# Optimization experiments

Hardware: AMD Instinct MI355X
Metric: run time of the kernel (lower is better)

## Reference

```python
import jax, jax.numpy as jnp
import numpy as np

N = 50000      # nodes
E = 800000     # edges (avg degree 16)
D_IN = 16      # raw node feature dim
D = 64         # d_model
H = 8          # heads
DH = D // H    # dim_head = 8
L = 2          # num_encoder_layers
EPS = 1e-5
SCALE = float(np.sqrt(DH))


def _xavier(key, shape):
    fan_in, fan_out = shape[-2], shape[-1]
    a = float(np.sqrt(6.0 / (fan_in + fan_out)))
    return jax.random.uniform(key, shape, jnp.float32, -a, a)


def setup_inputs() -> dict:
    key = jax.random.key(0)
    ks = jax.random.split(key, 20)
    feat = jax.random.normal(ks[0], (N, D_IN), jnp.float32)
    src = jax.random.randint(ks[1], (E,), 0, N, jnp.int32)
    dst = jax.random.randint(ks[2], (E,), 0, N, jnp.int32)
    return {
        "feat": feat,
        "src": src,
        "dst": dst,
        "W_emb": _xavier(ks[3], (D_IN, D)),
        "b_emb": jnp.zeros((D,), jnp.float32),
        "Wq": _xavier(ks[4], (L, D, D)),
        "Wk": _xavier(ks[5], (L, D, D)),
        "Wv": _xavier(ks[6], (L, D, D)),
        "Wo": _xavier(ks[7], (L, D, D)),
        "bo": jnp.zeros((L, D), jnp.float32),
        "bn1_g": jnp.ones((L, D), jnp.float32),
        "bn1_b": jnp.zeros((L, D), jnp.float32),
        "W1": _xavier(ks[8], (L, D, 2 * D)),
        "b1": jnp.zeros((L, 2 * D), jnp.float32),
        "W2": _xavier(ks[9], (L, 2 * D, D)),
        "b2": jnp.zeros((L, D), jnp.float32),
        "bn2_g": jnp.ones((L, D), jnp.float32),
        "bn2_b": jnp.zeros((L, D), jnp.float32),
    }


def _batch_norm(x, g, b):
    # BatchNorm1d (training-mode forward: batch statistics, biased var)
    mu = jnp.mean(x, axis=0)
    var = jnp.var(x, axis=0)
    return (x - mu) / jnp.sqrt(var + EPS) * g + b


def _layer(h, src, dst, Wq, Wk, Wv, Wo, bo, bn1_g, bn1_b, W1, b1, W2, b2, bn2_g, bn2_b):
    h_in1 = h
    Q = (h @ Wq).reshape(N, H, DH)
    K = (h @ Wk).reshape(N, H, DH)
    V = (h @ Wv).reshape(N, H, DH)
    # SDDMM: per-edge dot(K[src], Q[dst]) -> [E, H]
    e = jnp.sum(K[src] * Q[dst], axis=-1)
    # scaled_exp: exp(clamp(score/sqrt(dh), -10, 10)) stored as edge 'score'
    e = jnp.exp(jnp.clip(e / SCALE, -10.0, 10.0))
    # reduce_func then applies a softmax over mailbox scores (double exp, faithful)
    m = jax.ops.segment_max(e, dst, num_segments=N)          # [N, H]
    w = jnp.exp(e - m[dst])                                   # [E, H]
    s = jax.ops.segment_sum(w, dst, num_segments=N)           # [N, H]
    alpha = w / s[dst]                                        # [E, H]
    out = jax.ops.segment_sum(alpha[:, :, None] * V[src], dst, num_segments=N)
    h = out.reshape(N, D) @ Wo + bo
    h = _batch_norm(h_in1 + h, bn1_g, bn1_b)
    h_in2 = h
    h = jax.nn.relu(h @ W1 + b1) @ W2 + b2
    h = _batch_norm(h + h_in2, bn2_g, bn2_b)
    return h


def reference(feat, src, dst, W_emb, b_emb, Wq, Wk, Wv, Wo, bo, bn1_g, bn1_b,
              W1, b1, W2, b2, bn2_g, bn2_b):
    h = feat @ W_emb + b_emb  # embedding_h (dropout=0)
    for l in range(L):
        h = _layer(h, src, dst, Wq[l], Wk[l], Wv[l], Wo[l], bo[l],
                   bn1_g[l], bn1_b[l], W1[l], b1[l], W2[l], b2[l],
                   bn2_g[l], bn2_b[l])
    return h
```

## Files before the change

### kernel.cpp

```cpp
#include <hip/hip_runtime.h>

#define NNODES 50000
#define NEDGES 800000
#define DM 64
#define NH 8
#define DH 8
#define EPSN 1e-5f
#define INV_SCALE 0.3535533905932738f
#define SCAN_BLOCKS 200
#define SCAN_CHUNK  250

template<int KA, int KB, int R, bool RELU, bool RES, bool STATS, bool BNRES>
__global__ __launch_bounds__(256, 2) void gemm_k(const float* __restrict__ A,
    const float* __restrict__ W, int woff,
    const float* __restrict__ bias, int boff,
    float* __restrict__ C, float* __restrict__ stats,
    const float* __restrict__ bnstats, const float* __restrict__ bng, int bgoff,
    const float* __restrict__ bnb, int bboff, int Nrows)
{
    constexpr int CG   = KB / 4;
    constexpr int RG   = 256 / CG;
    constexpr int ROWS = RG * R;
    constexpr int APAD = KA + 4;
    constexpr int KAq  = KA / 4;

    __shared__ __align__(16) float sW[KA * KB];
    __shared__ __align__(16) float sA[ROWS * APAD];

    const int tid  = threadIdx.x;
    const int row0 = blockIdx.x * ROWS;

    for (int i4 = tid; i4 < KA * KB / 4; i4 += 256)
        *(float4*)&sW[i4 * 4] = ((const float4*)(W + woff))[i4];
    for (int i4 = tid; i4 < ROWS * KAq; i4 += 256) {
        int r = i4 / KAq, kq = i4 - r * KAq;
        int gr = row0 + r;
        float4 v = make_float4(0.f, 0.f, 0.f, 0.f);
        if (gr < Nrows) v = ((const float4*)A)[(size_t)gr * KAq + kq];
        *(float4*)&sA[r * APAD + kq * 4] = v;
    }
    __syncthreads();

    const int cg = tid % CG, rg = tid / CG;
    const int c0 = cg * 4, r0 = rg * R;

    float4 acc[R];
#pragma unroll
    for (int rr = 0; rr < R; rr++) acc[rr] = make_float4(0.f, 0.f, 0.f, 0.f);

#pragma unroll 2
    for (int k = 0; k < KA; k += 4) {
        float4 w0 = *(const float4*)&sW[(k + 0) * KB + c0];
        float4 w1 = *(const float4*)&sW[(k + 1) * KB + c0];
        float4 w2 = *(const float4*)&sW[(k + 2) * KB + c0];
        float4 w3 = *(const float4*)&sW[(k + 3) * KB + c0];
#pragma unroll
        for (int rr = 0; rr < R; rr++) {
            float4 av = *(const float4*)&sA[(r0 + rr) * APAD + k];
            acc[rr].x += av.x * w0.x + av.y * w1.x + av.z * w2.x + av.w * w3.x;
            acc[rr].y += av.x * w0.y + av.y * w1.y + av.z * w2.y + av.w * w3.y;
            acc[rr].z += av.x * w0.z + av.y * w1.z + av.z * w2.z + av.w * w3.z;
            acc[rr].w += av.x * w0.w + av.y * w1.w + av.z * w2.w + av.w * w3.w;
        }
    }

    float4 bv = make_float4(0.f, 0.f, 0.f, 0.f);
    if (bias) {
        bv.x = bias[boff + c0];     bv.y = bias[boff + c0 + 1];
        bv.z = bias[boff + c0 + 2]; bv.w = bias[boff + c0 + 3];
    }

    float4 scR = make_float4(1.f, 1.f, 1.f, 1.f);
    float4 ofR = make_float4(0.f, 0.f, 0.f, 0.f);
    if (BNRES) {
        const float inv_n = 1.0f / NNODES;
#pragma unroll
        for (int j = 0; j < 4; j++) {
            float mu   = bnstats[c0 + j] * inv_n;
            float var  = bnstats[KB + c0 + j] * inv_n - mu * mu;
            float istd = rsqrtf(fmaxf(var, 0.f) + EPSN);
            float s    = istd * bng[bgoff + c0 + j];
            ((float*)&scR)[j] = s;
            ((float*)&ofR)[j] = bnb[bboff + c0 + j] - mu * s;
        }
    }

    float4 vals[R];
#pragma unroll
    for (int rr = 0; rr < R; rr++) {
        int grow = row0 + r0 + rr;
        bool valid = grow < Nrows;
        float4 v;
        v.x = acc[rr].x + bv.x; v.y = acc[rr].y + bv.y;
        v.z = acc[rr].z + bv.z; v.w = acc[rr].w + bv.w;
        if (RELU) {
            v.x = fmaxf(v.x, 0.f); v.y = fmaxf(v.y, 0.f);
            v.z = fmaxf(v.z, 0.f); v.w = fmaxf(v.w, 0.f);
        }
        if (valid) {
            if (RES) {
                float4 old = *(const float4*)&C[(size_t)grow * KB + c0];
                if (BNRES) {
                    old.x = old.x * scR.x + ofR.x;
                    old.y = old.y * scR.y + ofR.y;
                    old.z = old.z * scR.z + ofR.z;
                    old.w = old.w * scR.w + ofR.w;
                }
                v.x += old.x; v.y += old.y; v.z += old.z; v.w += old.w;
            }
            *(float4*)&C[(size_t)grow * KB + c0] = v;
        } else {
            v = make_float4(0.f, 0.f, 0.f, 0.f);
        }
        vals[rr] = v;
    }

    if (STATS) {
        __syncthreads();
        float4 cs = make_float4(0.f, 0.f, 0.f, 0.f);
#pragma unroll
        for (int rr = 0; rr < R; rr++) {
            cs.x += vals[rr].x; cs.y += vals[rr].y;
            cs.z += vals[rr].z; cs.w += vals[rr].w;
        }
        *(float4*)&sA[rg * KB + c0] = cs;
        __syncthreads();
        if (tid < KB) {
            float s = 0.f;
#pragma unroll
            for (int g = 0; g < RG; g++) s += sA[g * KB + tid];
            atomicAdd(&stats[tid], s);
        }
        __syncthreads();
        float4 cq = make_float4(0.f, 0.f, 0.f, 0.f);
#pragma unroll
        for (int rr = 0; rr < R; rr++) {
            cq.x += vals[rr].x * vals[rr].x; cq.y += vals[rr].y * vals[rr].y;
            cq.z += vals[rr].z * vals[rr].z; cq.w += vals[rr].w * vals[rr].w;
        }
        *(float4*)&sA[rg * KB + c0] = cq;
        __syncthreads();
        if (tid < KB) {
            float s = 0.f;
#pragma unroll
            for (int g = 0; g < RG; g++) s += sA[g * KB + tid];
            atomicAdd(&stats[KB + tid], s);
        }
    }
}

template<bool BNIN>
__global__ __launch_bounds__(256, 2) void qkv_k(const float* __restrict__ A,
    const float* __restrict__ Wq, const float* __restrict__ Wk,
    const float* __restrict__ Wv, int woff,
    float* __restrict__ Qo, float* __restrict__ Ko, float* __restrict__ Vo,
    const float* __restrict__ bnstats, const float* __restrict__ bng, int bgoff,
    const float* __restrict__ bnb, int bboff, int Nrows)
{
    constexpr int APAD = 68;
    __shared__ __align__(16) float sW[64 * 64];
    __shared__ __align__(16) float sA[64 * APAD];

    const int tid  = threadIdx.x;
    const int row0 = blockIdx.x * 64;

    {
        const int kq = tid & 15, cc = kq * 4;
        float4 sc = make_float4(1.f, 1.f, 1.f, 1.f);
        float4 of = make_float4(0.f, 0.f, 0.f, 0.f);
        if (BNIN) {
            const float inv_n = 1.0f / NNODES;
#pragma unroll
            for (int j = 0; j < 4; j++) {
                float mu   = bnstats[cc + j] * inv_n;
                float var  = bnstats[64 + cc + j] * inv_n - mu * mu;
                float istd = rsqrtf(fmaxf(var, 0.f) + EPSN);
                float s    = istd * bng[bgoff + cc + j];
                ((float*)&sc)[j] = s;
                ((float*)&of)[j] = bnb[bboff + cc + j] - mu * s;
            }
        }
        for (int i4 = tid; i4 < 64 * 16; i4 += 256) {
            int r = i4 >> 4;
            int gr = row0 + r;
            float4 v = make_float4(0.f, 0.f, 0.f, 0.f);
            if (gr < Nrows) {
                v = ((const float4*)A)[(size_t)gr * 16 + kq];
                if (BNIN) {
                    v.x = v.x * sc.x + of.x; v.y = v.y * sc.y + of.y;
                    v.z = v.z * sc.z + of.z; v.w = v.w * sc.w + of.w;
                }
            }
            *(float4*)&sA[r * APAD + cc] = v;
        }
    }

    const float* Ws[3]   = {Wq, Wk, Wv};
    float*       Outs[3] = {Qo, Ko, Vo};

    const int cg = tid & 15, rg = tid >> 4;
    const int c0 = cg * 4, r0 = rg * 4;

    for (int m = 0; m < 3; m++) {
        __syncthreads();
        for (int i4 = tid; i4 < 1024; i4 += 256)
            *(float4*)&sW[i4 * 4] = ((const float4*)(Ws[m] + woff))[i4];
        __syncthreads();

        float4 acc[4];
#pragma unroll
        for (int rr = 0; rr < 4; rr++) acc[rr] = make_float4(0.f, 0.f, 0.f, 0.f);

#pragma unroll 2
        for (int k = 0; k < 64; k += 4) {
            float4 w0 = *(const float4*)&sW[(k + 0) * 64 + c0];
            float4 w1 = *(const float4*)&sW[(k + 1) * 64 + c0];
            float4 w2 = *(const float4*)&sW[(k + 2) * 64 + c0];
            float4 w3 = *(const float4*)&sW[(k + 3) * 64 + c0];
#pragma unroll
            for (int rr = 0; rr < 4; rr++) {
                float4 av = *(const float4*)&sA[(r0 + rr) * APAD + k];
                acc[rr].x += av.x * w0.x + av.y * w1.x + av.z * w2.x + av.w * w3.x;
                acc[rr].y += av.x * w0.y + av.y * w1.y + av.z * w2.y + av.w * w3.y;
                acc[rr].z += av.x * w0.z + av.y * w1.z + av.z * w2.z + av.w * w3.z;
                acc[rr].w += av.x * w0.w + av.y * w1.w + av.z * w2.w + av.w * w3.w;
            }
        }

#pragma unroll
        for (int rr = 0; rr < 4; rr++) {
            int grow = row0 + r0 + rr;
            if (grow < Nrows)
                *(float4*)&Outs[m][(size_t)grow * 64 + c0] = acc[rr];
        }
    }
}

__global__ __launch_bounds__(256, 4) void ffn_k(float* __restrict__ H,
    const float* __restrict__ W1, int w1off,
    const float* __restrict__ b1, int b1off,
    const float* __restrict__ W2, int w2off,
    const float* __restrict__ b2, int b2off,
    const float* __restrict__ bnstats,
    const float* __restrict__ bng, int bgoff,
    const float* __restrict__ bnb, int bboff,
    float* __restrict__ stats2, int Nrows)
{
    constexpr int APAD = 68;
    __shared__ __align__(16) float sA[4][8 * APAD];
    __shared__ __align__(16) float sF[4][8 * 128];
    __shared__ __align__(16) float sR[4 * 64];

    const int tid  = threadIdx.x;
    const int w    = tid >> 6;
    const int c    = tid & 63;
    const int row0 = blockIdx.x * 32 + w * 8;

    float* sAw = sA[w];
    float* sFw = sF[w];
    const float* __restrict__ W1g = W1 + w1off;
    const float* __restrict__ W2g = W2 + w2off;

    {
        const int q = c & 15;
        const int r = c >> 4;
        const float inv_n = 1.0f / NNODES;
        float4 sc, of;
#pragma unroll
        for (int j = 0; j < 4; j++) {
            float mu   = bnstats[q * 4 + j] * inv_n;
            float var  = bnstats[64 + q * 4 + j] * inv_n - mu * mu;
            float istd = rsqrtf(fmaxf(var, 0.f) + EPSN);
            float s    = istd * bng[bgoff + q * 4 + j];
            ((float*)&sc)[j] = s;
            ((float*)&of)[j] = bnb[bboff + q * 4 + j] - mu * s;
        }
#pragma unroll
        for (int rr = 0; rr < 2; rr++) {
            int lr = r + rr * 4;
            int gr = row0 + lr;
            float4 v = make_float4(0.f, 0.f, 0.f, 0.f);
            if (gr < Nrows) {
                v = ((const float4*)H)[(size_t)gr * 16 + q];
                v.x = v.x * sc.x + of.x; v.y = v.y * sc.y + of.y;
                v.z = v.z * sc.z + of.z; v.w = v.w * sc.w + of.w;
            }
            *(float4*)&sAw[lr * APAD + q * 4] = v;
        }
    }

    {
        float accL[8], accH[8];
#pragma unroll
        for (int r = 0; r < 8; r++) { accL[r] = 0.f; accH[r] = 0.f; }
#pragma unroll 2
        for (int k4 = 0; k4 < 16; k4++) {
            float4 av[8];
#pragma unroll
            for (int r = 0; r < 8; r++)
                av[r] = *(const float4*)&sAw[r * APAD + k4 * 4];
#pragma unroll
            for (int j = 0; j < 4; j++) {
                int k = k4 * 4 + j;
                float wl = W1g[k * 128 + c];
                float wh = W1g[k * 128 + c + 64];
#pragma unroll
                for (int r = 0; r < 8; r++) {
                    float a = ((const float*)&av[r])[j];
                    accL[r] += a * wl;
                    accH[r] += a * wh;
                }
            }
        }
        float bL = b1[b1off + c], bH = b1[b1off + c + 64];
#pragma unroll
        for (int r = 0; r < 8; r++) {
            sFw[r * 128 + c]      = fmaxf(accL[r] + bL, 0.f);
            sFw[r * 128 + c + 64] = fmaxf(accH[r] + bH, 0.f);
        }
    }

    float acc2[8];
#pragma unroll
    for (int r = 0; r < 8; r++) acc2[r] = 0.f;
#pragma unroll 2
    for (int k4 = 0; k4 < 32; k4++) {
        float4 fv[8];
#pragma unroll
        for (int r = 0; r < 8; r++)
            fv[r] = *(const float4*)&sFw[r * 128 + k4 * 4];
#pragma unroll
        for (int j = 0; j < 4; j++) {
            int k = k4 * 4 + j;
            float w2 = W2g[k * 64 + c];
#pragma unroll
            for (int r = 0; r < 8; r++)
                acc2[r] += ((const float*)&fv[r])[j] * w2;
        }
    }

    const float bc = b2[b2off + c];
    float vals[8];
#pragma unroll
    for (int r = 0; r < 8; r++) {
        int grow = row0 + r;
        float v = acc2[r] + bc + sAw[r * APAD + c];
        if (grow < Nrows) H[(size_t)grow * 64 + c] = v;
        else v = 0.f;
        vals[r] = v;
    }

    float s = 0.f, qsum = 0.f;
#pragma unroll
    for (int r = 0; r < 8; r++) { s += vals[r]; qsum += vals[r] * vals[r]; }
    sR[w * 64 + c] = s;
    __syncthreads();
    if (tid < 64) {
        float t = sR[tid] + sR[64 + tid] + sR[128 + tid] + sR[192 + tid];
        atomicAdd(&stats2[tid], t);
    }
    __syncthreads();
    sR[w * 64 + c] = qsum;
    __syncthreads();
    if (tid < 64) {
        float t = sR[tid] + sR[64 + tid] + sR[128 + tid] + sR[192 + tid];
        atomicAdd(&stats2[64 + tid], t);
    }
}

__global__ __launch_bounds__(256) void bn_apply(const float* __restrict__ Hin,
    float* __restrict__ Hout, const float* __restrict__ stats,
    const float* __restrict__ g, int goff, const float* __restrict__ b, int boff)
{
    int i = blockIdx.x * 256 + threadIdx.x;
    if (i >= NNODES * DM) return;
    int c = i & 63;
    float mu  = stats[c] * (1.0f / NNODES);
    float var = stats[64 + c] * (1.0f / NNODES) - mu * mu;
    float istd = rsqrtf(fmaxf(var, 0.0f) + EPSN);
    Hout[i] = (Hin[i] - mu) * istd * g[goff + c] + b[boff + c];
}

__global__ __launch_bounds__(256) void zero_int_k(int* __restrict__ p, int n)
{
    int i = blockIdx.x * 256 + threadIdx.x;
    if (i < n) p[i] = 0;
}

__global__ __launch_bounds__(256) void count_k(const int* __restrict__ dst,
                                               int* __restrict__ cursor)
{
    int e = blockIdx.x * 256 + threadIdx.x;
    if (e < NEDGES) atomicAdd(&cursor[dst[e]], 1);
}

__global__ __launch_bounds__(256) void csr_scanA(const int* __restrict__ cursor,
                                                 int* __restrict__ bsum)
{
    __shared__ int red[256];
    const int base = blockIdx.x * SCAN_CHUNK;
    int s = 0;
    for (int i = threadIdx.x; i < SCAN_CHUNK; i += 256) s += cursor[base + i];
    red[threadIdx.x] = s;
    __syncthreads();
    for (int o = 128; o > 0; o >>= 1) {
        if (threadIdx.x < o) red[threadIdx.x] += red[threadIdx.x + o];
        __syncthreads();
    }
    if (threadIdx.x == 0) bsum[blockIdx.x] = red[0];
}

__global__ __launch_bounds__(256) void csr_scanB(int* __restrict__ bsum)
{
    __shared__ int t[256];
    const int tid = threadIdx.x;
    int v = (tid < SCAN_BLOCKS) ? bsum[tid] : 0;
    t[tid] = v;
    __syncthreads();
    for (int off = 1; off < 256; off <<= 1) {
        int x = (tid >= off) ? t[tid - off] : 0;
        __syncthreads();
        t[tid] += x;
        __syncthreads();
    }
    if (tid < SCAN_BLOCKS) bsum[tid] = t[tid] - v;
}

__global__ __launch_bounds__(256) void csr_scanC(int* __restrict__ cursor,
    int* __restrict__ rowptr, const int* __restrict__ bsum)
{
    __shared__ int t[256];
    const int base = blockIdx.x * SCAN_CHUNK;
    const int tid  = threadIdx.x;
    int deg = (tid < SCAN_CHUNK) ? cursor[base + tid] : 0;
    t[tid] = deg;
    __syncthreads();
    for (int off = 1; off < 256; off <<= 1) {
        int x = (tid >= off) ? t[tid - off] : 0;
        __syncthreads();
        t[tid] += x;
        __syncthreads();
    }
    int excl = bsum[blockIdx.x] + t[tid] - deg;
    if (tid < SCAN_CHUNK) {
        rowptr[base + tid] = excl;
        cursor[base + tid] = excl;
    }
    if (blockIdx.x == 0 && tid == 0) rowptr[NNODES] = NEDGES;
}

__global__ __launch_bounds__(256) void fill_k(const int* __restrict__ src,
    const int* __restrict__ dst, int* __restrict__ cursor,
    int* __restrict__ nbr)
{
    int e = blockIdx.x * 256 + threadIdx.x;
    if (e >= NEDGES) return;
    int pos = atomicAdd(&cursor[dst[e]], 1);
    nbr[pos] = src[e];
}

__global__ __launch_bounds__(256) void attn_fused_k(const float* __restrict__ Q,
    const float* __restrict__ K, const float* __restrict__ V,
    const int* __restrict__ rowptr, const int* __restrict__ nbr,
    float* __restrict__ U)
{
    const int w = threadIdx.x >> 6;
    const int d = blockIdx.x * 4 + w;
    if (d >= NNODES) return;
    const int l  = threadIdx.x & 63;
    const int el = l >> 3;
    const int h  = l & 7;
    const int e0 = rowptr[d], e1 = rowptr[d + 1];
    const int deg = e1 - e0;

    if (deg == 0) {
        U[(size_t)d * DM + h * DH + el] = 0.f;
        return;
    }

    const float4* qp = (const float4*)(Q + (size_t)d * DM + h * DH);
    const float4 q0 = qp[0], q1 = qp[1];

    float m = 0.0f;
    float S = 0.0f;
    float u[8] = {0.f, 0.f, 0.f, 0.f, 0.f, 0.f, 0.f, 0.f};

    for (int base = 0; base < deg; base += 16) {
        const int i0 = base + el, i1 = base + 8 + el;
        const bool v0ok = i0 < deg, v1ok = i1 < deg;
        const int s0 = nbr[e0 + (v0ok ? i0 : 0)];
        const int s1 = nbr[e0 + (v1ok ? i1 : 0)];

        const float4* kp0 = (const float4*)(K + (size_t)s0 * DM + h * DH);
        const float4* vp0 = (const float4*)(V + (size_t)s0 * DM + h * DH);
        const float4* kp1 = (const float4*)(K + (size_t)s1 * DM + h * DH);
        const float4* vp1 = (const float4*)(V + (size_t)s1 * DM + h * DH);
        float4 ka0 = kp0[0], ka1 = kp0[1];
        float4 kb0 = kp1[0], kb1 = kp1[1];
        float4 va0 = vp0[0], va1 = vp0[1];
        float4 vb0 = vp1[0], vb1 = vp1[1];

        float d0 = ka0.x * q0.x + ka0.y * q0.y + ka0.z * q0.z + ka0.w * q0.w
                 + ka1.x * q1.x + ka1.y * q1.y + ka1.z * q1.z + ka1.w * q1.w;
        float d1 = kb0.x * q0.x + kb0.y * q0.y + kb0.z * q0.z + kb0.w * q0.w
                 + kb1.x * q1.x + kb1.y * q1.y + kb1.z * q1.z + kb1.w * q1.w;

        float ev0 = __expf(fminf(fmaxf(d0 * INV_SCALE, -10.f), 10.f));
        float ev1 = __expf(fminf(fmaxf(d1 * INV_SCALE, -10.f), 10.f));
        if (!v0ok) ev0 = 0.f;
        if (!v1ok) ev1 = 0.f;

        float bm = fmaxf(ev0, ev1);
        bm = fmaxf(bm, __shfl_xor(bm, 8, 64));
        bm = fmaxf(bm, __shfl_xor(bm, 16, 64));
        bm = fmaxf(bm, __shfl_xor(bm, 32, 64));

        const float mn = fmaxf(m, bm);
        const float r  = __expf(m - mn);
        const float w0 = v0ok ? __expf(ev0 - mn) : 0.f;
        const float w1 = v1ok ? __expf(ev1 - mn) : 0.f;

        S = S * r + w0 + w1;
        u[0] = u[0] * r + w0 * va0.x + w1 * vb0.x;
        u[1] = u[1] * r + w0 * va0.y + w1 * vb0.y;
        u[2] = u[2] * r + w0 * va0.z + w1 * vb0.z;
        u[3] = u[3] * r + w0 * va0.w + w1 * vb0.w;
        u[4] = u[4] * r + w0 * va1.x + w1 * vb1.x;
        u[5] = u[5] * r + w0 * va1.y + w1 * vb1.y;
        u[6] = u[6] * r + w0 * va1.z + w1 * vb1.z;
        u[7] = u[7] * r + w0 * va1.w + w1 * vb1.w;
        m = mn;
    }

#pragma unroll
    for (int off = 8; off <= 32; off <<= 1) {
        S += __shfl_xor(S, off, 64);
#pragma unroll
        for (int j = 0; j < 8; j++) u[j] += __shfl_xor(u[j], off, 64);
    }

    const float out = (S > 0.f) ? u[el] / S : 0.f;
    U[(size_t)d * DM + h * DH + el] = out;
}

__global__ __launch_bounds__(256) void fill_const_k(float* __restrict__ out, int n)
{
    int i = blockIdx.x * 256 + threadIdx.x;
    if (i < n) out[i] = 100.0f;
}

extern "C" void kernel_launch(void* const* d_in, const int* in_sizes, int n_in,
                              void* d_out, int out_size, void* d_ws, size_t ws_size,
                              hipStream_t stream)
{
    const int expect[18] = {800000, 800000, 800000, 1024, 64,
                            8192, 8192, 8192, 8192, 128,
                            128, 128, 16384, 256, 16384, 128, 128, 128};
    bool order_ok = (n_in == 18) && (out_size == NNODES * DM);
    if (order_ok)
        for (int i = 0; i < 18; i++)
            if (in_sizes[i] != expect[i]) { order_ok = false; break; }
    if (!order_ok) {
        fill_const_k<<<(out_size + 255) / 256, 256, 0, stream>>>((float*)d_out,
                                                                 out_size);
        return;
    }

    const float* feat  = (const float*)d_in[0];
    const int*   src   = (const int*)d_in[1];
    const int*   dst   = (const int*)d_in[2];
    const float* W_emb = (const float*)d_in[3];
    const float* b_emb = (const float*)d_in[4];
    const float* Wq    = (const float*)d_in[5];
    const float* Wk    = (const float*)d_in[6];
    const float* Wv    = (const float*)d_in[7];
    const float* Wo    = (const float*)d_in[8];
    const float* bo    = (const float*)d_in[9];
    const float* bn1_g = (const float*)d_in[10];
    const float* bn1_b = (const float*)d_in[11];
    const float* W1    = (const float*)d_in[12];
    const float* b1    = (const float*)d_in[13];
    const float* W2    = (const float*)d_in[14];
    const float* b2    = (const float*)d_in[15];
    const float* bn2_g = (const float*)d_in[16];
    const float* bn2_b = (const float*)d_in[17];

    const size_t ND = (size_t)NNODES * DM;
    float* ws     = (float*)d_ws;
    float* Hb     = ws;
    float* Qb     = Hb + ND;
    float* Kb     = Qb + ND;
    float* Vb     = Kb + ND;
    float* Ub     = Vb + ND;
    float* stats  = Ub + ND;
    int*   rowptr = (int*)(stats + 256);
    int*   cursor = rowptr + (NNODES + 1);
    int*   bsum   = cursor + NNODES;
    int*   nbr    = bsum + SCAN_BLOCKS;

    float* statsA = stats;
    float* statsB = stats + 128;

    const size_t BASE = (5 * ND + 256) * 4
                      + ((NNODES + 1) + NNODES + SCAN_BLOCKS + NEDGES) * 4;
    if (ws_size < BASE) {
        fill_const_k<<<(out_size + 255) / 256, 256, 0, stream>>>((float*)d_out,
                                                                 out_size);
        return;
    }

    const int g64 = (NNODES + 63) / 64;
    const int g32 = (NNODES + 31) / 32;
    const int gND = (int)(ND / 256);
    const int gE  = (NEDGES + 255) / 256;
    const int gAT = (NNODES + 3) / 4;

    zero_int_k<<<(NNODES + 255) / 256, 256, 0, stream>>>(cursor, NNODES);
    count_k<<<gE, 256, 0, stream>>>(dst, cursor);
    csr_scanA<<<SCAN_BLOCKS, 256, 0, stream>>>(cursor, bsum);
    csr_scanB<<<1, 256, 0, stream>>>(bsum);
    csr_scanC<<<SCAN_BLOCKS, 256, 0, stream>>>(cursor, rowptr, bsum);
    fill_k<<<gE, 256, 0, stream>>>(src, dst, cursor, nbr);

    gemm_k<16, 64, 4, false, false, false, false>
        <<<g64, 256, 0, stream>>>(feat, W_emb, 0, b_emb, 0, Hb, nullptr,
                                  nullptr, nullptr, 0, nullptr, 0, NNODES);

    for (int l = 0; l < 2; l++) {
        const int woff  = l * DM * DM;
        const int w1off = l * DM * 2 * DM;
        const int boff  = l * DM;
        const int b1off = l * 2 * DM;
        const int poff  = (l - 1) * DM;

        if (l == 0)
            qkv_k<false><<<g64, 256, 0, stream>>>(Hb, Wq, Wk, Wv, woff,
                Qb, Kb, Vb, nullptr, nullptr, 0, nullptr, 0, NNODES);
        else
            qkv_k<true><<<g64, 256, 0, stream>>>(Hb, Wq, Wk, Wv, woff,
                Qb, Kb, Vb, statsB, bn2_g, poff, bn2_b, poff, NNODES);

        attn_fused_k<<<gAT, 256, 0, stream>>>(Qb, Kb, Vb, rowptr, nbr, Ub);

        hipMemsetAsync(statsA, 0, 128 * 4, stream);
        if (l == 0)
            gemm_k<64, 64, 4, false, true, true, false>
                <<<g64, 256, 0, stream>>>(Ub, Wo, woff, bo, boff, Hb, statsA,
                                          nullptr, nullptr, 0, nullptr, 0, NNODES);
        else
            gemm_k<64, 64, 4, false, true, true, true>
                <<<g64, 256, 0, stream>>>(Ub, Wo, woff, bo, boff, Hb, statsA,
                                          statsB, bn2_g, poff, bn2_b, poff, NNODES);

        hipMemsetAsync(statsB, 0, 128 * 4, stream);
        ffn_k<<<g32, 256, 0, stream>>>(Hb, W1, w1off, b1, b1off,
                                       W2, w1off, b2, boff,
                                       statsA, bn1_g, boff, bn1_b, boff,
                                       statsB, NNODES);
    }

    bn_apply<<<gND, 256, 0, stream>>>(Hb, (float*)d_out, statsB,
                                      bn2_g, DM, bn2_b, DM);
}
```

Before: 567.0 us.

## Remap FFN kernel threads to row-by-column-quad with float4 weight loads

Restructures the fused FFN kernel so each lane owns one row and four adjacent output columns, not one column across eight rows. Weight reads become float4 vector loads, the hidden buffer gets padding, and the per-column stats reduction uses wavefront shuffles with a single barrier and one combined atomic pass. This aims to cut global load instruction count and barrier overhead, but gives up the reuse of each weight value across eight rows. Per-thread weight traffic therefore rises, and the BN scale/offset is now recomputed per element.

```diff
diff --git a/kernel.cpp b/kernel.cpp
--- a/kernel.cpp
+++ b/kernel.cpp
@@ -247,124 +247,123 @@
     float* __restrict__ stats2, int Nrows)
 {
     constexpr int APAD = 68;
-    __shared__ __align__(16) float sA[4][8 * APAD];
-    __shared__ __align__(16) float sF[4][8 * 128];
-    __shared__ __align__(16) float sR[4 * 64];
+    constexpr int FPAD = 132;
+    __shared__ __align__(16) float smem[2176 + 4224 + 512];
 
     const int tid  = threadIdx.x;
     const int w    = tid >> 6;
-    const int c    = tid & 63;
+    const int lane = tid & 63;
+    const int r    = lane >> 3;
+    const int j    = lane & 7;
     const int row0 = blockIdx.x * 32 + w * 8;
-
-    float* sAw = sA[w];
-    float* sFw = sF[w];
+    const int grow = row0 + r;
+    const bool rv  = grow < Nrows;
+
+    float* sAw = smem + w * (8 * APAD);
+    float* sFw = smem + 2176 + w * (8 * FPAD);
+    float* sR  = smem + 2176 + 4224;
+
     const float* __restrict__ W1g = W1 + w1off;
     const float* __restrict__ W2g = W2 + w2off;
 
     {
-        const int q = c & 15;
-        const int r = c >> 4;
         const float inv_n = 1.0f / NNODES;
-        float4 sc, of;
-#pragma unroll
-        for (int j = 0; j < 4; j++) {
-            float mu   = bnstats[q * 4 + j] * inv_n;
-            float var  = bnstats[64 + q * 4 + j] * inv_n - mu * mu;
-            float istd = rsqrtf(fmaxf(var, 0.f) + EPSN);
-            float s    = istd * bng[bgoff + q * 4 + j];
-            ((float*)&sc)[j] = s;
-            ((float*)&of)[j] = bnb[bboff + q * 4 + j] - mu * s;
-        }
-#pragma unroll
-        for (int rr = 0; rr < 2; rr++) {
-            int lr = r + rr * 4;
-            int gr = row0 + lr;
+#pragma unroll
+        for (int t = 0; t < 2; t++) {
+            const int q = j + t * 8;
             float4 v = make_float4(0.f, 0.f, 0.f, 0.f);
-            if (gr < Nrows) {
-                v = ((const float4*)H)[(size_t)gr * 16 + q];
-                v.x = v.x * sc.x + of.x; v.y = v.y * sc.y + of.y;
-                v.z = v.z * sc.z + of.z; v.w = v.w * sc.w + of.w;
-            }
-            *(float4*)&sAw[lr * APAD + q * 4] = v;
-        }
-    }
-
-    {
-        float accL[8], accH[8];
-#pragma unroll
-        for (int r = 0; r < 8; r++) { accL[r] = 0.f; accH[r] = 0.f; }
-#pragma unroll 2
-        for (int k4 = 0; k4 < 16; k4++) {
-            float4 av[8];
-#pragma unroll
-            for (int r = 0; r < 8; r++)
-                av[r] = *(const float4*)&sAw[r * APAD + k4 * 4];
-#pragma unroll
-            for (int j = 0; j < 4; j++) {
-                int k = k4 * 4 + j;
-                float wl = W1g[k * 128 + c];
-                float wh = W1g[k * 128 + c + 64];
-#pragma unroll
-                for (int r = 0; r < 8; r++) {
-                    float a = ((const float*)&av[r])[j];
-                    accL[r] += a * wl;
-                    accH[r] += a * wh;
+            if (rv) {
+                v = ((const float4*)H)[(size_t)grow * 16 + q];
+#pragma unroll
+                for (int jj = 0; jj < 4; jj++) {
+                    float mu   = bnstats[q * 4 + jj] * inv_n;
+                    float var  = bnstats[64 + q * 4 + jj] * inv_n - mu * mu;
+                    float istd = rsqrtf(fmaxf(var, 0.f) + EPSN);
+                    float s    = istd * bng[bgoff + q * 4 + jj];
+                    ((float*)&v)[jj] = ((float*)&v)[jj] * s
+                                     + (bnb[bboff + q * 4 + jj] - mu * s);
                 }
             }
-        }
-        float bL = b1[b1off + c], bH = b1[b1off + c + 64];
-#pragma unroll
-        for (int r = 0; r < 8; r++) {
-            sFw[r * 128 + c]      = fmaxf(accL[r] + bL, 0.f);
-            sFw[r * 128 + c + 64] = fmaxf(accH[r] + bH, 0.f);
-        }
-    }
-
-    float acc2[8];
-#pragma unroll
-    for (int r = 0; r < 8; r++) acc2[r] = 0.f;
-#pragma unroll 2
-    for (int k4 = 0; k4 < 32; k4++) {
-        float4 fv[8];
-#pragma unroll
-        for (int r = 0; r < 8; r++)
-            fv[r] = *(const float4*)&sFw[r * 128 + k4 * 4];
-#pragma unroll
-        for (int j = 0; j < 4; j++) {
-            int k = k4 * 4 + j;
-            float w2 = W2g[k * 64 + c];
-#pragma unroll
-            for (int r = 0; r < 8; r++)
-                acc2[r] += ((const float*)&fv[r])[j] * w2;
-        }
-    }
-
-    const float bc = b2[b2off + c];
-    float vals[8];
-#pragma unroll
-    for (int r = 0; r < 8; r++) {
-        int grow = row0 + r;
-        float v = acc2[r] + bc + sAw[r * APAD + c];
-        if (grow < Nrows) H[(size_t)grow * 64 + c] = v;
-        else v = 0.f;
-        vals[r] = v;
-    }
-
-    float s = 0.f, qsum = 0.f;
-#pragma unroll
-    for (int r = 0; r < 8; r++) { s += vals[r]; qsum += vals[r] * vals[r]; }
-    sR[w * 64 + c] = s;
+            *(float4*)&sAw[r * APAD + q * 4] = v;
+        }
+    }
+
+#pragma unroll
+    for (int p = 0; p < 4; p++) {
+        const int c0 = p * 32 + j * 4;
+        float4 acc = make_float4(0.f, 0.f, 0.f, 0.f);
+#pragma unroll 4
+        for (int k4 = 0; k4 < 16; k4++) {
+            float4 a = *(const float4*)&sAw[r * APAD + k4 * 4];
+#pragma unroll
+            for (int kk = 0; kk < 4; kk++) {
+                float av = ((const float*)&a)[kk];
+                float4 wv = *(const float4*)&W1g[(k4 * 4 + kk) * 128 + c0];
+                acc.x += av * wv.x; acc.y += av * wv.y;
+                acc.z += av * wv.z; acc.w += av * wv.w;
+            }
+        }
+        float4 bb = *(const float4*)&b1[b1off + c0];
+        acc.x = fmaxf(acc.x + bb.x, 0.f);
+        acc.y = fmaxf(acc.y + bb.y, 0.f);
+        acc.z = fmaxf(acc.z + bb.z, 0.f);
+        acc.w = fmaxf(acc.w + bb.w, 0.f);
+        *(float4*)&sFw[r * FPAD + c0] = acc;
+    }
+
+    float4 outv[2];
+#pragma unroll
+    for (int p = 0; p < 2; p++) {
+        const int c0 = p * 32 + j * 4;
+        float4 acc = make_float4(0.f, 0.f, 0.f, 0.f);
+#pragma unroll 4
+        for (int k4 = 0; k4 < 32; k4++) {
+            float4 f = *(const float4*)&sFw[r * FPAD + k4 * 4];
+#pragma unroll
+            for (int kk = 0; kk < 4; kk++) {
+                float fv = ((const float*)&f)[kk];
+                float4 wv = *(const float4*)&W2g[(k4 * 4 + kk) * 64 + c0];
+                acc.x += fv * wv.x; acc.y += fv * wv.y;
+                acc.z += fv * wv.z; acc.w += fv * wv.w;
+            }
+        }
+        float4 bb  = *(const float4*)&b2[b2off + c0];
+        float4 res = *(const float4*)&sAw[r * APAD + c0];
+        float4 v;
+        v.x = acc.x + bb.x + res.x;
+        v.y = acc.y + bb.y + res.y;
+        v.z = acc.z + bb.z + res.z;
+        v.w = acc.w + bb.w + res.w;
+        if (rv) *(float4*)&H[(size_t)grow * 64 + c0] = v;
+        else    v = make_float4(0.f, 0.f, 0.f, 0.f);
+        outv[p] = v;
+    }
+
+    float4 s0 = outv[0], s1 = outv[1];
+    float4 q0, q1;
+    q0.x = s0.x * s0.x; q0.y = s0.y * s0.y; q0.z = s0.z * s0.z; q0.w = s0.w * s0.w;
+    q1.x = s1.x * s1.x; q1.y = s1.y * s1.y; q1.z = s1.z * s1.z; q1.w = s1.w * s1.w;
+#pragma unroll
+    for (int off = 8; off <= 32; off <<= 1) {
+        s0.x += __shfl_xor(s0.x, off, 64); s0.y += __shfl_xor(s0.y, off, 64);
+        s0.z += __shfl_xor(s0.z, off, 64); s0.w += __shfl_xor(s0.w, off, 64);
+        s1.x += __shfl_xor(s1.x, off, 64); s1.y += __shfl_xor(s1.y, off, 64);
+        s1.z += __shfl_xor(s1.z, off, 64); s1.w += __shfl_xor(s1.w, off, 64);
+        q0.x += __shfl_xor(q0.x, off, 64); q0.y += __shfl_xor(q0.y, off, 64);
+        q0.z += __shfl_xor(q0.z, off, 64); q0.w += __shfl_xor(q0.w, off, 64);
+        q1.x += __shfl_xor(q1.x, off, 64); q1.y += __shfl_xor(q1.y, off, 64);
+        q1.z += __shfl_xor(q1.z, off, 64); q1.w += __shfl_xor(q1.w, off, 64);
+    }
+    if (r == 0) {
+        *(float4*)&sR[w * 128 + j * 4]      = s0;
+        *(float4*)&sR[w * 128 + 32 + j * 4] = s1;
+        *(float4*)&sR[w * 128 + 64 + j * 4] = q0;
+        *(float4*)&sR[w * 128 + 96 + j * 4] = q1;
+    }
     __syncthreads();
-    if (tid < 64) {
-        float t = sR[tid] + sR[64 + tid] + sR[128 + tid] + sR[192 + tid];
+    if (tid < 128) {
+        float t = sR[tid] + sR[128 + tid] + sR[256 + tid] + sR[384 + tid];
         atomicAdd(&stats2[tid], t);
-    }
-    __syncthreads();
-    sR[w * 64 + c] = qsum;
-    __syncthreads();
-    if (tid < 64) {
-        float t = sR[tid] + sR[64 + tid] + sR[128 + tid] + sR[192 + tid];
-        atomicAdd(&stats2[64 + tid], t);
     }
 }
 
```

Result: slower. 662.5 us (+16.9%).
